# Performance work log

Measured on AMD Instinct MI355X. Metric: run time of the kernel, lower is better.

## Reference

```python
import jax, jax.numpy as jnp
import numpy as np

B, L_IN, T = 1024, 512, 96
IN_DIM, OUT_DIM = 1, 1
H_ENC, H_DEC = 128, 256  # decoder hidden = 2 * encoder hidden (bidir concat)


def _lstm_cell(x, h, c, Wih, Whh, b):
    # PyTorch gate order: i, f, g, o. b = b_ih + b_hh (equivalent to two biases).
    gates = x @ Wih.T + h @ Whh.T + b
    i, f, g, o = jnp.split(gates, 4, axis=-1)
    c = jax.nn.sigmoid(f) * c + jax.nn.sigmoid(i) * jnp.tanh(g)
    h = jax.nn.sigmoid(o) * jnp.tanh(c)
    return h, c


def _lstm_final(xs, Wih, Whh, b, hidden, reverse=False):
    # xs: [L, B, D]; returns final (h, c) only (encoder outputs are unused).
    h0 = jnp.zeros((xs.shape[1], hidden), xs.dtype)
    c0 = jnp.zeros((xs.shape[1], hidden), xs.dtype)

    def step(carry, x):
        h, c = _lstm_cell(x, carry[0], carry[1], Wih, Whh, b)
        return (h, c), None

    (h, c), _ = jax.lax.scan(step, (h0, c0), xs, reverse=reverse)
    return h, c


def setup_inputs() -> dict:
    key = jax.random.key(0)
    ks = jax.random.split(key, 13)
    p = lambda k, s: (jax.random.normal(k, s, jnp.float32) * 0.05)
    return {
        "source": jax.random.normal(ks[0], (B, L_IN, IN_DIM), jnp.float32),
        "target_tensor": jnp.zeros((B, T, OUT_DIM), jnp.float32),
        "enc_Wih_f": p(ks[1], (4 * H_ENC, IN_DIM)),
        "enc_Whh_f": p(ks[2], (4 * H_ENC, H_ENC)),
        "enc_b_f": p(ks[3], (4 * H_ENC,)),
        "enc_Wih_b": p(ks[4], (4 * H_ENC, IN_DIM)),
        "enc_Whh_b": p(ks[5], (4 * H_ENC, H_ENC)),
        "enc_b_b": p(ks[6], (4 * H_ENC,)),
        "dec_Wih": p(ks[7], (4 * H_DEC, OUT_DIM)),
        "dec_Whh": p(ks[8], (4 * H_DEC, H_DEC)),
        "dec_b": p(ks[9], (4 * H_DEC,)),
        "out_W": p(ks[10], (OUT_DIM, H_DEC)),
        "out_b": p(ks[11], (OUT_DIM,)),
    }


def reference(source, target_tensor, enc_Wih_f, enc_Whh_f, enc_b_f,
              enc_Wih_b, enc_Whh_b, enc_b_b,
              dec_Wih, dec_Whh, dec_b, out_W, out_b):
    batch = source.shape[0]
    t_len = target_tensor.shape[1]
    out_dim = target_tensor.shape[-1]

    xs = jnp.swapaxes(source, 0, 1)  # [L, B, IN]
    h_f, c_f = _lstm_final(xs, enc_Wih_f, enc_Whh_f, enc_b_f, H_ENC, reverse=False)
    h_b, c_b = _lstm_final(xs, enc_Wih_b, enc_Whh_b, enc_b_b, H_ENC, reverse=True)
    h0 = jnp.concatenate([h_f, h_b], axis=-1)  # [B, 2*H_ENC]
    c0 = jnp.concatenate([c_f, c_b], axis=-1)

    y0 = jnp.zeros((batch, out_dim), source.dtype)

    def dec_step(carry, _):
        h, c, y = carry
        h, c = _lstm_cell(y, h, c, dec_Wih, dec_Whh, dec_b)
        y = h @ out_W.T + out_b
        return (h, c, y), y

    _, ys = jax.lax.scan(dec_step, (h0, c0, y0), None, length=t_len)
    return jnp.swapaxes(ys, 0, 1)  # [B, T, OUT]
```

## Files before the change

### kernel.cpp

```cpp
#include <hip/hip_runtime.h>
#include <math.h>

#define H_ENC 128
#define H_DEC 256
#define L_SRC 512
#define T_DEC 96
#define B_TOT 1024

typedef _Float16 half8 __attribute__((ext_vector_type(8)));
typedef float f32x4 __attribute__((ext_vector_type(4)));

#define MFMA16(A, B, C) __builtin_amdgcn_mfma_f32_16x16x32_f16((A), (B), (C), 0, 0, 0)

__device__ __forceinline__ unsigned packu(float a, float b) {
    union { _Float16 h[2]; unsigned u; } x; x.h[0] = (_Float16)a; x.h[1] = (_Float16)b; return x.u;
}

__device__ __forceinline__ float sigmoidf_(float x) {
    return __builtin_amdgcn_rcpf(1.f + __expf(-x));
}
__device__ __forceinline__ float tanhf_(float x) {
    return 1.f - 2.f * __builtin_amdgcn_rcpf(__expf(2.f * x) + 1.f);
}

#define CNT_STRIDE 104
__global__ void zero_cnt(int* cnt) {
    int i = blockIdx.x * blockDim.x + threadIdx.x;
    if (i < 64 * CNT_STRIDE) cnt[i] = 0;
}

#define EB 4
#define HPAD 136
__global__ __launch_bounds__(512, 4)
void encoder_eb4r(
    const float* __restrict__ source,
    const float* __restrict__ Wih_f, const float* __restrict__ Whh_f, const float* __restrict__ b_f,
    const float* __restrict__ Wih_b, const float* __restrict__ Whh_b, const float* __restrict__ b_b,
    float* __restrict__ h0, float* __restrict__ c0)
{
    const int dir = blockIdx.x & 1;
    const int bg  = blockIdx.x >> 1;
    const int t   = threadIdx.x;
    const int w   = t >> 6;
    const int l   = t & 63;
    const int col = l & 15;
    const int grp = l >> 4;

    const float* Wih = dir ? Wih_b : Wih_f;
    const float* Whh = dir ? Whh_b : Whh_f;
    const float* bb  = dir ? b_b   : b_f;

    __shared__ float    xsT[L_SRC][EB];
    __shared__ _Float16 hbuf[2][EB][HPAD];
    __shared__ float    gbuf[4][EB][H_ENC];

    {
        const float* srcb = source + (size_t)bg * EB * L_SRC;
        for (int i = t; i < EB * L_SRC; i += 512) {
            int b = i >> 9, st = i & 511;
            xsT[st][b] = srcb[i];
        }
        for (int i = t; i < 2 * EB * HPAD; i += 512)
            ((_Float16*)hbuf)[i] = (_Float16)0.f;
    }

    half8 wf[4][4];
    #pragma unroll
    for (int tau = 0; tau < 4; ++tau) {
        const int n = 4 * w + tau;
        const int grow = (n >> 3) * H_ENC + 16 * (n & 7) + col;
        const float* wr = Whh + (size_t)grow * H_ENC;
        #pragma unroll
        for (int kt = 0; kt < 4; ++kt) {
            const float* p = wr + 32 * kt + 8 * grp;
            float4 v0 = *reinterpret_cast<const float4*>(p);
            float4 v1 = *reinterpret_cast<const float4*>(p + 4);
            half8 h;
            h[0] = (_Float16)v0.x; h[1] = (_Float16)v0.y; h[2] = (_Float16)v0.z; h[3] = (_Float16)v0.w;
            h[4] = (_Float16)v1.x; h[5] = (_Float16)v1.y; h[6] = (_Float16)v1.z; h[7] = (_Float16)v1.w;
            wf[tau][kt] = h;
        }
    }

    const int ub = t >> 7;
    const int ue = t & 127;
    const float bI = bb[ue],           wI = Wih[ue];
    const float bF = bb[H_ENC + ue],   wF = Wih[H_ENC + ue];
    const float bG = bb[2*H_ENC + ue], wG = Wih[2*H_ENC + ue];
    const float bO = bb[3*H_ENC + ue], wO = Wih[3*H_ENC + ue];

    float c = 0.f, hlast = 0.f;
    __syncthreads();

    int cur = 0;
    for (int s = 0; s < L_SRC; ++s) {
        const int step = dir ? (L_SRC - 1 - s) : s;

        half8 a0 = {0,0,0,0,0,0,0,0}, a1 = a0, a2 = a0, a3 = a0;
        if (col < EB) {
            a0 = *reinterpret_cast<const half8*>(&hbuf[cur][col][ 0 + 8 * grp]);
            a1 = *reinterpret_cast<const half8*>(&hbuf[cur][col][32 + 8 * grp]);
            a2 = *reinterpret_cast<const half8*>(&hbuf[cur][col][64 + 8 * grp]);
            a3 = *reinterpret_cast<const half8*>(&hbuf[cur][col][96 + 8 * grp]);
        }

        f32x4 acc0 = {0.f, 0.f, 0.f, 0.f};
        f32x4 acc1 = {0.f, 0.f, 0.f, 0.f};
        f32x4 acc2 = {0.f, 0.f, 0.f, 0.f};
        f32x4 acc3 = {0.f, 0.f, 0.f, 0.f};
        acc0 = MFMA16(a0, wf[0][0], acc0); acc0 = MFMA16(a1, wf[0][1], acc0);
        acc0 = MFMA16(a2, wf[0][2], acc0); acc0 = MFMA16(a3, wf[0][3], acc0);
        acc1 = MFMA16(a0, wf[1][0], acc1); acc1 = MFMA16(a1, wf[1][1], acc1);
        acc1 = MFMA16(a2, wf[1][2], acc1); acc1 = MFMA16(a3, wf[1][3], acc1);
        acc2 = MFMA16(a0, wf[2][0], acc2); acc2 = MFMA16(a1, wf[2][1], acc2);
        acc2 = MFMA16(a2, wf[2][2], acc2); acc2 = MFMA16(a3, wf[2][3], acc2);
        acc3 = MFMA16(a0, wf[3][0], acc3); acc3 = MFMA16(a1, wf[3][1], acc3);
        acc3 = MFMA16(a2, wf[3][2], acc3); acc3 = MFMA16(a3, wf[3][3], acc3);

        if (grp == 0) {
            #pragma unroll
            for (int tau = 0; tau < 4; ++tau) {
                const int n = 4 * w + tau;
                const int G = n >> 3;
                const int e = 16 * (n & 7) + col;
                const f32x4 acc = (tau == 0) ? acc0 : (tau == 1) ? acc1 : (tau == 2) ? acc2 : acc3;
                #pragma unroll
                for (int r = 0; r < 4; ++r)
                    gbuf[G][r][e] = acc[r];
            }
        }
        __syncthreads();

        {
            float x = xsT[step][ub];
            float gi = sigmoidf_(gbuf[0][ub][ue] + bI + wI * x);
            float gf = sigmoidf_(gbuf[1][ub][ue] + bF + wF * x);
            float gg = tanhf_  (gbuf[2][ub][ue] + bG + wG * x);
            float go = sigmoidf_(gbuf[3][ub][ue] + bO + wO * x);
            c = gf * c + gi * gg;
            float h = go * tanhf_(c);
            hlast = h;
            hbuf[cur ^ 1][ub][ue] = (_Float16)h;
        }
        __syncthreads();
        cur ^= 1;
    }

    h0[(size_t)(bg * EB + ub) * (2 * H_ENC) + dir * H_ENC + ue] = hlast;
    c0[(size_t)(bg * EB + ub) * (2 * H_ENC) + dir * H_ENC + ue] = c;
}

#define DB 16
__global__ __launch_bounds__(512, 2)
void decoder_split(
    const float* __restrict__ Wih,
    const float* __restrict__ bb,
    const float* __restrict__ outW,
    const float* __restrict__ outb,
    const float* __restrict__ h0,
    const float* __restrict__ c0,
    const float* __restrict__ Whh,
    unsigned* __restrict__ hx,
    int* __restrict__ cnt,
    float* __restrict__ out)
{
    const int blk = blockIdx.x;
    const int bg  = blk & 63;
    const int q   = blk >> 6;
    const int t   = threadIdx.x;
    const int w   = t >> 6;
    const int l   = t & 63;
    const int col = l & 15;
    const int grp = l >> 4;
    const int u   = w >> 1;
    const int fo  = w & 1;

    __shared__ unsigned hlU[DB][132];
    __shared__ float    exch[4][2][DB][16];
    __shared__ unsigned hnewU[DB][32];
    __shared__ float    yl[DB];
    __shared__ float    owl[H_DEC];
    int* mycnt = cnt + bg * CNT_STRIDE;

    if (t < H_DEC) owl[t] = outW[t];

    const int j0 = 64 * q + 16 * u + col;
    const int rA = (fo ? 256 : 0) + j0;
    const int rB = (fo ? 768 : 512) + j0;

    half8 wfA[8], wfB[8];
    #pragma unroll
    for (int kt = 0; kt < 8; ++kt) {
        const float* pa = Whh + (size_t)rA * H_DEC + 32 * kt + 8 * grp;
        const float* pb = Whh + (size_t)rB * H_DEC + 32 * kt + 8 * grp;
        float4 a0 = *reinterpret_cast<const float4*>(pa);
        float4 a1 = *reinterpret_cast<const float4*>(pa + 4);
        float4 b0 = *reinterpret_cast<const float4*>(pb);
        float4 b1 = *reinterpret_cast<const float4*>(pb + 4);
        half8 ha, hb;
        ha[0]=(_Float16)a0.x; ha[1]=(_Float16)a0.y; ha[2]=(_Float16)a0.z; ha[3]=(_Float16)a0.w;
        ha[4]=(_Float16)a1.x; ha[5]=(_Float16)a1.y; ha[6]=(_Float16)a1.z; ha[7]=(_Float16)a1.w;
        hb[0]=(_Float16)b0.x; hb[1]=(_Float16)b0.y; hb[2]=(_Float16)b0.z; hb[3]=(_Float16)b0.w;
        hb[4]=(_Float16)b1.x; hb[5]=(_Float16)b1.y; hb[6]=(_Float16)b1.z; hb[7]=(_Float16)b1.w;
        wfA[kt] = ha; wfB[kt] = hb;
    }

    const float bI = bb[j0],       wI = Wih[j0];
    const float bF = bb[256 + j0], wF = Wih[256 + j0];
    const float bG = bb[512 + j0], wG = Wih[512 + j0];
    const float bO = bb[768 + j0], wO = Wih[768 + j0];
    const float ob = outb[0];

    float c[4];
    #pragma unroll
    for (int r = 0; r < 4; ++r)
        c[r] = c0[(size_t)(bg * DB + 4 * grp + r) * H_DEC + j0];

    {
        int batch = t >> 5, pair = t & 31;
        int e = 64 * q + 2 * pair;
        const float* hp = h0 + (size_t)(bg * DB + batch) * H_DEC + e;
        unsigned v = packu(hp[0], hp[1]);
        __hip_atomic_store(&hx[(size_t)(bg * DB + batch) * 128 + 32 * q + pair], v,
                           __ATOMIC_RELAXED, __HIP_MEMORY_SCOPE_AGENT);
    }
    __syncthreads();
    if (t == 0) {
        __hip_atomic_fetch_add(&mycnt[0], 1, __ATOMIC_RELAXED, __HIP_MEMORY_SCOPE_AGENT);
        while (__hip_atomic_load(&mycnt[0], __ATOMIC_RELAXED, __HIP_MEMORY_SCOPE_AGENT) < 4)
            __builtin_amdgcn_s_sleep(1);
    }
    __syncthreads();

    for (int s = 1; s <= T_DEC; ++s) {
        const int rb = (s - 1) & 1, wb = s & 1;
        #pragma unroll
        for (int i = 0; i < 4; ++i) {
            int j = t + 512 * i;
            int batch = j >> 7, within = j & 127;
            unsigned v = __hip_atomic_load(
                &hx[(size_t)rb * (B_TOT * 128) + (size_t)(bg * DB + batch) * 128 + within],
                __ATOMIC_RELAXED, __HIP_MEMORY_SCOPE_AGENT);
            hlU[batch][within] = v;
        }
        __syncthreads();

        {
            int batch = t >> 5, seg = t & 31;
            half8 hv = *reinterpret_cast<const half8*>(
                reinterpret_cast<const char*>(hlU) + batch * 528 + seg * 16);
            float sum = 0.f;
            #pragma unroll
            for (int j = 0; j < 8; ++j) sum += (float)hv[j] * owl[8 * seg + j];
            #pragma unroll
            for (int m = 1; m < 32; m <<= 1) sum += __shfl_xor(sum, m);
            if (seg == 0) {
                float yv = sum + ob;
                yl[batch] = (s == 1) ? 0.f : yv;
                if (q == 0 && s >= 2) out[(size_t)(bg * DB + batch) * T_DEC + (s - 2)] = yv;
            }
        }

        half8 a[8];
        #pragma unroll
        for (int kt = 0; kt < 8; ++kt)
            a[kt] = *reinterpret_cast<const half8*>(
                reinterpret_cast<const char*>(hlU) + col * 528 + (32 * kt + 8 * grp) * 2);

        f32x4 accA = {0.f, 0.f, 0.f, 0.f};
        f32x4 accB = {0.f, 0.f, 0.f, 0.f};
        #pragma unroll
        for (int kt = 0; kt < 8; ++kt) {
            accA = MFMA16(a[kt], wfA[kt], accA);
            accB = MFMA16(a[kt], wfB[kt], accB);
        }

        if (fo) {
            #pragma unroll
            for (int r = 0; r < 4; ++r) {
                exch[u][0][4 * grp + r][col] = accA[r] + bF;
                exch[u][1][4 * grp + r][col] = accB[r] + bO;
            }
        }
        __syncthreads();

        if (!fo) {
            #pragma unroll
            for (int r = 0; r < 4; ++r) {
                float yb = yl[4 * grp + r];
                float gi = sigmoidf_(accA[r] + bI + wI * yb);
                float gg = tanhf_  (accB[r] + bG + wG * yb);
                float gf = sigmoidf_(exch[u][0][4 * grp + r][col] + wF * yb);
                float go = sigmoidf_(exch[u][1][4 * grp + r][col] + wO * yb);
                c[r] = gf * c[r] + gi * gg;
                float h = go * tanhf_(c[r]);
                reinterpret_cast<_Float16*>(hnewU)[(4 * grp + r) * 64 + 16 * u + col] = (_Float16)h;
            }
        }
        __syncthreads();

        {
            int batch = t >> 5, pair = t & 31;
            __hip_atomic_store(
                &hx[(size_t)wb * (B_TOT * 128) + (size_t)(bg * DB + batch) * 128 + 32 * q + pair],
                hnewU[batch][pair], __ATOMIC_RELAXED, __HIP_MEMORY_SCOPE_AGENT);
        }
        __syncthreads();
        if (t == 0) {
            __hip_atomic_fetch_add(&mycnt[s], 1, __ATOMIC_RELAXED, __HIP_MEMORY_SCOPE_AGENT);
            while (__hip_atomic_load(&mycnt[s], __ATOMIC_RELAXED, __HIP_MEMORY_SCOPE_AGENT) < 4)
                __builtin_amdgcn_s_sleep(1);
        }
        __syncthreads();
    }

    {
        #pragma unroll
        for (int i = 0; i < 4; ++i) {
            int j = t + 512 * i;
            int batch = j >> 7, within = j & 127;
            unsigned v = __hip_atomic_load(
                &hx[(size_t)(bg * DB + batch) * 128 + within],
                __ATOMIC_RELAXED, __HIP_MEMORY_SCOPE_AGENT);
            hlU[batch][within] = v;
        }
        __syncthreads();
        int batch = t >> 5, seg = t & 31;
        half8 hv = *reinterpret_cast<const half8*>(
            reinterpret_cast<const char*>(hlU) + batch * 528 + seg * 16);
        float sum = 0.f;
        #pragma unroll
        for (int j = 0; j < 8; ++j) sum += (float)hv[j] * owl[8 * seg + j];
        #pragma unroll
        for (int m = 1; m < 32; m <<= 1) sum += __shfl_xor(sum, m);
        if (q == 0 && seg == 0)
            out[(size_t)(bg * DB + batch) * T_DEC + (T_DEC - 1)] = sum + ob;
    }
}

extern "C" void kernel_launch(void* const* d_in, const int* in_sizes, int n_in,
                              void* d_out, int out_size, void* d_ws, size_t ws_size,
                              hipStream_t stream) {
    const float* source = (const float*)d_in[0];
    const float* eWih_f = (const float*)d_in[2];
    const float* eWhh_f = (const float*)d_in[3];
    const float* eb_f   = (const float*)d_in[4];
    const float* eWih_b = (const float*)d_in[5];
    const float* eWhh_b = (const float*)d_in[6];
    const float* eb_b   = (const float*)d_in[7];
    const float* dWih   = (const float*)d_in[8];
    const float* dWhh   = (const float*)d_in[9];
    const float* db     = (const float*)d_in[10];
    const float* oW     = (const float*)d_in[11];
    const float* obp    = (const float*)d_in[12];
    float* out = (float*)d_out;

    float*    h0  = (float*)d_ws;
    float*    c0  = h0 + (size_t)B_TOT * H_DEC;
    unsigned* hx  = (unsigned*)(c0 + (size_t)B_TOT * H_DEC);
    int*      cnt = (int*)(hx + (size_t)2 * B_TOT * 128);

    zero_cnt<<<(64 * CNT_STRIDE + 255) / 256, 256, 0, stream>>>(cnt);
    encoder_eb4r<<<256 * 2, 512, 0, stream>>>(
        source, eWih_f, eWhh_f, eb_f, eWih_b, eWhh_b, eb_b, h0, c0);
    decoder_split<<<256, 512, 0, stream>>>(
        dWih, db, oW, obp, h0, c0, dWhh, hx, cnt, out);
}
```

Measured before the change: 822.6 us.

## Process four batch chunks per decoder block and fold encoder bias into MFMA

The decoder now launches 64 blocks instead of 256, and each block loops over four 16-batch chunks that share the register-resident weight fragments. The cross-block counter barrier moves to the start of each step, so a block only waits before it reads hidden state. In the encoder, the bias is used as the initial MFMA accumulator instead of being added in the gate math. Both kernels raise wave priority around the MFMA chains. Fewer blocks lowers barrier and launch overhead but serialises four chunks per block, which may lengthen each step.

```diff
diff --git a/kernel.cpp b/kernel.cpp
--- a/kernel.cpp
+++ b/kernel.cpp
@@ -65,10 +65,12 @@
     }
 
     half8 wf[4][4];
+    float bias4[4];
     #pragma unroll
     for (int tau = 0; tau < 4; ++tau) {
         const int n = 4 * w + tau;
         const int grow = (n >> 3) * H_ENC + 16 * (n & 7) + col;
+        bias4[tau] = bb[grow];
         const float* wr = Whh + (size_t)grow * H_ENC;
         #pragma unroll
         for (int kt = 0; kt < 4; ++kt) {
@@ -84,10 +86,10 @@
 
     const int ub = t >> 7;
     const int ue = t & 127;
-    const float bI = bb[ue],           wI = Wih[ue];
-    const float bF = bb[H_ENC + ue],   wF = Wih[H_ENC + ue];
-    const float bG = bb[2*H_ENC + ue], wG = Wih[2*H_ENC + ue];
-    const float bO = bb[3*H_ENC + ue], wO = Wih[3*H_ENC + ue];
+    const float wI = Wih[ue];
+    const float wF = Wih[H_ENC + ue];
+    const float wG = Wih[2*H_ENC + ue];
+    const float wO = Wih[3*H_ENC + ue];
 
     float c = 0.f, hlast = 0.f;
     __syncthreads();
@@ -104,10 +106,11 @@
             a3 = *reinterpret_cast<const half8*>(&hbuf[cur][col][96 + 8 * grp]);
         }
 
-        f32x4 acc0 = {0.f, 0.f, 0.f, 0.f};
-        f32x4 acc1 = {0.f, 0.f, 0.f, 0.f};
-        f32x4 acc2 = {0.f, 0.f, 0.f, 0.f};
-        f32x4 acc3 = {0.f, 0.f, 0.f, 0.f};
+        f32x4 acc0 = {bias4[0], bias4[0], bias4[0], bias4[0]};
+        f32x4 acc1 = {bias4[1], bias4[1], bias4[1], bias4[1]};
+        f32x4 acc2 = {bias4[2], bias4[2], bias4[2], bias4[2]};
+        f32x4 acc3 = {bias4[3], bias4[3], bias4[3], bias4[3]};
+        __builtin_amdgcn_s_setprio(1);
         acc0 = MFMA16(a0, wf[0][0], acc0); acc0 = MFMA16(a1, wf[0][1], acc0);
         acc0 = MFMA16(a2, wf[0][2], acc0); acc0 = MFMA16(a3, wf[0][3], acc0);
         acc1 = MFMA16(a0, wf[1][0], acc1); acc1 = MFMA16(a1, wf[1][1], acc1);
@@ -116,6 +119,7 @@
         acc2 = MFMA16(a2, wf[2][2], acc2); acc2 = MFMA16(a3, wf[2][3], acc2);
         acc3 = MFMA16(a0, wf[3][0], acc3); acc3 = MFMA16(a1, wf[3][1], acc3);
         acc3 = MFMA16(a2, wf[3][2], acc3); acc3 = MFMA16(a3, wf[3][3], acc3);
+        __builtin_amdgcn_s_setprio(0);
 
         if (grp == 0) {
             #pragma unroll
@@ -133,10 +137,10 @@
 
         {
             float x = xsT[step][ub];
-            float gi = sigmoidf_(gbuf[0][ub][ue] + bI + wI * x);
-            float gf = sigmoidf_(gbuf[1][ub][ue] + bF + wF * x);
-            float gg = tanhf_  (gbuf[2][ub][ue] + bG + wG * x);
-            float go = sigmoidf_(gbuf[3][ub][ue] + bO + wO * x);
+            float gi = sigmoidf_(gbuf[0][ub][ue] + wI * x);
+            float gf = sigmoidf_(gbuf[1][ub][ue] + wF * x);
+            float gg = tanhf_  (gbuf[2][ub][ue] + wG * x);
+            float go = sigmoidf_(gbuf[3][ub][ue] + wO * x);
             c = gf * c + gi * gg;
             float h = go * tanhf_(c);
             hlast = h;
@@ -151,8 +155,9 @@
 }
 
 #define DB 16
+#define NCH 4
 __global__ __launch_bounds__(512, 2)
-void decoder_split(
+void decoder_mc(
     const float* __restrict__ Wih,
     const float* __restrict__ bb,
     const float* __restrict__ outW,
@@ -165,8 +170,8 @@
     float* __restrict__ out)
 {
     const int blk = blockIdx.x;
-    const int bg  = blk & 63;
-    const int q   = blk >> 6;
+    const int G2  = blk & 15;
+    const int q   = blk >> 4;
     const int t   = threadIdx.x;
     const int w   = t >> 6;
     const int l   = t & 63;
@@ -175,12 +180,12 @@
     const int u   = w >> 1;
     const int fo  = w & 1;
 
-    __shared__ unsigned hlU[DB][132];
+    __shared__ unsigned hlU[NCH][DB][132];
     __shared__ float    exch[4][2][DB][16];
     __shared__ unsigned hnewU[DB][32];
-    __shared__ float    yl[DB];
+    __shared__ float    yl[NCH][DB];
     __shared__ float    owl[H_DEC];
-    int* mycnt = cnt + bg * CNT_STRIDE;
+    int* mycnt = cnt + (size_t)(G2 * NCH) * CNT_STRIDE;
 
     if (t < H_DEC) owl[t] = outW[t];
 
@@ -211,12 +216,18 @@
     const float bO = bb[768 + j0], wO = Wih[768 + j0];
     const float ob = outb[0];
 
-    float c[4];
-    #pragma unroll
-    for (int r = 0; r < 4; ++r)
-        c[r] = c0[(size_t)(bg * DB + 4 * grp + r) * H_DEC + j0];
-
-    {
+    float c[NCH][4];
+    #pragma unroll
+    for (int ch = 0; ch < NCH; ++ch) {
+        const int bg = G2 * NCH + ch;
+        #pragma unroll
+        for (int r = 0; r < 4; ++r)
+            c[ch][r] = c0[(size_t)(bg * DB + 4 * grp + r) * H_DEC + j0];
+    }
+
+    #pragma unroll
+    for (int ch = 0; ch < NCH; ++ch) {
+        const int bg = G2 * NCH + ch;
         int batch = t >> 5, pair = t & 31;
         int e = 64 * q + 2 * pair;
         const float* hp = h0 + (size_t)(bg * DB + batch) * H_DEC + e;
@@ -225,116 +236,131 @@
                            __ATOMIC_RELAXED, __HIP_MEMORY_SCOPE_AGENT);
     }
     __syncthreads();
-    if (t == 0) {
-        __hip_atomic_fetch_add(&mycnt[0], 1, __ATOMIC_RELAXED, __HIP_MEMORY_SCOPE_AGENT);
-        while (__hip_atomic_load(&mycnt[0], __ATOMIC_RELAXED, __HIP_MEMORY_SCOPE_AGENT) < 4)
-            __builtin_amdgcn_s_sleep(1);
-    }
-    __syncthreads();
+    if (t < NCH)
+        __hip_atomic_fetch_add(&mycnt[(size_t)t * CNT_STRIDE + 0], 1,
+                               __ATOMIC_RELAXED, __HIP_MEMORY_SCOPE_AGENT);
 
     for (int s = 1; s <= T_DEC; ++s) {
         const int rb = (s - 1) & 1, wb = s & 1;
-        #pragma unroll
-        for (int i = 0; i < 4; ++i) {
-            int j = t + 512 * i;
-            int batch = j >> 7, within = j & 127;
-            unsigned v = __hip_atomic_load(
-                &hx[(size_t)rb * (B_TOT * 128) + (size_t)(bg * DB + batch) * 128 + within],
-                __ATOMIC_RELAXED, __HIP_MEMORY_SCOPE_AGENT);
-            hlU[batch][within] = v;
-        }
-        __syncthreads();
-
-        {
+
+        if (t < NCH) {
+            while (__hip_atomic_load(&mycnt[(size_t)t * CNT_STRIDE + (s - 1)],
+                                     __ATOMIC_RELAXED, __HIP_MEMORY_SCOPE_AGENT) < 4)
+                __builtin_amdgcn_s_sleep(1);
+        }
+        __syncthreads();
+
+        #pragma unroll
+        for (int i = 0; i < 16; ++i) {
+            int idx = t + 512 * i;
+            ((unsigned*)hlU)[(idx >> 7) * 132 + (idx & 127)] =
+                __hip_atomic_load(&hx[(size_t)rb * (B_TOT * 128) + (size_t)G2 * 8192 + idx],
+                                  __ATOMIC_RELAXED, __HIP_MEMORY_SCOPE_AGENT);
+        }
+        __syncthreads();
+
+        #pragma unroll
+        for (int ch = 0; ch < NCH; ++ch) {
+            const int bg = G2 * NCH + ch;
+            const char* hbase = reinterpret_cast<const char*>(hlU[ch]);
+
+            {
+                int batch = t >> 5, seg = t & 31;
+                half8 hv = *reinterpret_cast<const half8*>(hbase + batch * 528 + seg * 16);
+                float sum = 0.f;
+                #pragma unroll
+                for (int j = 0; j < 8; ++j) sum += (float)hv[j] * owl[8 * seg + j];
+                #pragma unroll
+                for (int m = 1; m < 32; m <<= 1) sum += __shfl_xor(sum, m);
+                if (seg == 0) {
+                    float yv = sum + ob;
+                    yl[ch][batch] = (s == 1) ? 0.f : yv;
+                    if (q == 0 && s >= 2) out[(size_t)(bg * DB + batch) * T_DEC + (s - 2)] = yv;
+                }
+            }
+
+            half8 a[8];
+            #pragma unroll
+            for (int kt = 0; kt < 8; ++kt)
+                a[kt] = *reinterpret_cast<const half8*>(hbase + col * 528 + (32 * kt + 8 * grp) * 2);
+
+            f32x4 accA = {0.f, 0.f, 0.f, 0.f};
+            f32x4 accB = {0.f, 0.f, 0.f, 0.f};
+            __builtin_amdgcn_s_setprio(1);
+            #pragma unroll
+            for (int kt = 0; kt < 8; ++kt) {
+                accA = MFMA16(a[kt], wfA[kt], accA);
+                accB = MFMA16(a[kt], wfB[kt], accB);
+            }
+            __builtin_amdgcn_s_setprio(0);
+
+            if (fo) {
+                #pragma unroll
+                for (int r = 0; r < 4; ++r) {
+                    exch[u][0][4 * grp + r][col] = accA[r] + bF;
+                    exch[u][1][4 * grp + r][col] = accB[r] + bO;
+                }
+            }
+            __syncthreads();
+
+            if (!fo) {
+                #pragma unroll
+                for (int r = 0; r < 4; ++r) {
+                    float yb = yl[ch][4 * grp + r];
+                    float gi = sigmoidf_(accA[r] + bI + wI * yb);
+                    float gg = tanhf_  (accB[r] + bG + wG * yb);
+                    float gf = sigmoidf_(exch[u][0][4 * grp + r][col] + wF * yb);
+                    float go = sigmoidf_(exch[u][1][4 * grp + r][col] + wO * yb);
+                    c[ch][r] = gf * c[ch][r] + gi * gg;
+                    float h = go * tanhf_(c[ch][r]);
+                    reinterpret_cast<_Float16*>(hnewU)[(4 * grp + r) * 64 + 16 * u + col] = (_Float16)h;
+                }
+            }
+            __syncthreads();
+
+            {
+                int batch = t >> 5, pair = t & 31;
+                __hip_atomic_store(
+                    &hx[(size_t)wb * (B_TOT * 128) + (size_t)(bg * DB + batch) * 128 + 32 * q + pair],
+                    hnewU[batch][pair], __ATOMIC_RELAXED, __HIP_MEMORY_SCOPE_AGENT);
+            }
+        }
+
+        __syncthreads();
+        if (t < NCH)
+            __hip_atomic_fetch_add(&mycnt[(size_t)t * CNT_STRIDE + s], 1,
+                                   __ATOMIC_RELAXED, __HIP_MEMORY_SCOPE_AGENT);
+    }
+
+    if (t < NCH) {
+        while (__hip_atomic_load(&mycnt[(size_t)t * CNT_STRIDE + T_DEC],
+                                 __ATOMIC_RELAXED, __HIP_MEMORY_SCOPE_AGENT) < 4)
+            __builtin_amdgcn_s_sleep(1);
+    }
+    __syncthreads();
+    #pragma unroll
+    for (int i = 0; i < 16; ++i) {
+        int idx = t + 512 * i;
+        ((unsigned*)hlU)[(idx >> 7) * 132 + (idx & 127)] =
+            __hip_atomic_load(&hx[(size_t)G2 * 8192 + idx],
+                              __ATOMIC_RELAXED, __HIP_MEMORY_SCOPE_AGENT);
+    }
+    __syncthreads();
+    if (q == 0) {
+        #pragma unroll
+        for (int ch = 0; ch < NCH; ++ch) {
+            const int bg = G2 * NCH + ch;
             int batch = t >> 5, seg = t & 31;
             half8 hv = *reinterpret_cast<const half8*>(
-                reinterpret_cast<const char*>(hlU) + batch * 528 + seg * 16);
+                reinterpret_cast<const char*>(hlU[ch]) + batch * 528 + seg * 16);
             float sum = 0.f;
             #pragma unroll
             for (int j = 0; j < 8; ++j) sum += (float)hv[j] * owl[8 * seg + j];
             #pragma unroll
             for (int m = 1; m < 32; m <<= 1) sum += __shfl_xor(sum, m);
-            if (seg == 0) {
-                float yv = sum + ob;
-                yl[batch] = (s == 1) ? 0.f : yv;
-                if (q == 0 && s >= 2) out[(size_t)(bg * DB + batch) * T_DEC + (s - 2)] = yv;
-            }
-        }
-
-        half8 a[8];
-        #pragma unroll
-        for (int kt = 0; kt < 8; ++kt)
-            a[kt] = *reinterpret_cast<const half8*>(
-                reinterpret_cast<const char*>(hlU) + col * 528 + (32 * kt + 8 * grp) * 2);
-
-        f32x4 accA = {0.f, 0.f, 0.f, 0.f};
-        f32x4 accB = {0.f, 0.f, 0.f, 0.f};
-        #pragma unroll
-        for (int kt = 0; kt < 8; ++kt) {
-            accA = MFMA16(a[kt], wfA[kt], accA);
-            accB = MFMA16(a[kt], wfB[kt], accB);
-        }
-
-        if (fo) {
-            #pragma unroll
-            for (int r = 0; r < 4; ++r) {
-                exch[u][0][4 * grp + r][col] = accA[r] + bF;
-                exch[u][1][4 * grp + r][col] = accB[r] + bO;
-            }
-        }
-        __syncthreads();
-
-        if (!fo) {
-            #pragma unroll
-            for (int r = 0; r < 4; ++r) {
-                float yb = yl[4 * grp + r];
-                float gi = sigmoidf_(accA[r] + bI + wI * yb);
-                float gg = tanhf_  (accB[r] + bG + wG * yb);
-                float gf = sigmoidf_(exch[u][0][4 * grp + r][col] + wF * yb);
-                float go = sigmoidf_(exch[u][1][4 * grp + r][col] + wO * yb);
-                c[r] = gf * c[r] + gi * gg;
-                float h = go * tanhf_(c[r]);
-                reinterpret_cast<_Float16*>(hnewU)[(4 * grp + r) * 64 + 16 * u + col] = (_Float16)h;
-            }
-        }
-        __syncthreads();
-
-        {
-            int batch = t >> 5, pair = t & 31;
-            __hip_atomic_store(
-                &hx[(size_t)wb * (B_TOT * 128) + (size_t)(bg * DB + batch) * 128 + 32 * q + pair],
-                hnewU[batch][pair], __ATOMIC_RELAXED, __HIP_MEMORY_SCOPE_AGENT);
-        }
-        __syncthreads();
-        if (t == 0) {
-            __hip_atomic_fetch_add(&mycnt[s], 1, __ATOMIC_RELAXED, __HIP_MEMORY_SCOPE_AGENT);
-            while (__hip_atomic_load(&mycnt[s], __ATOMIC_RELAXED, __HIP_MEMORY_SCOPE_AGENT) < 4)
-                __builtin_amdgcn_s_sleep(1);
-        }
-        __syncthreads();
-    }
-
-    {
-        #pragma unroll
-        for (int i = 0; i < 4; ++i) {
-            int j = t + 512 * i;
-            int batch = j >> 7, within = j & 127;
-            unsigned v = __hip_atomic_load(
-                &hx[(size_t)(bg * DB + batch) * 128 + within],
-                __ATOMIC_RELAXED, __HIP_MEMORY_SCOPE_AGENT);
-            hlU[batch][within] = v;
-        }
-        __syncthreads();
-        int batch = t >> 5, seg = t & 31;
-        half8 hv = *reinterpret_cast<const half8*>(
-            reinterpret_cast<const char*>(hlU) + batch * 528 + seg * 16);
-        float sum = 0.f;
-        #pragma unroll
-        for (int j = 0; j < 8; ++j) sum += (float)hv[j] * owl[8 * seg + j];
-        #pragma unroll
-        for (int m = 1; m < 32; m <<= 1) sum += __shfl_xor(sum, m);
-        if (q == 0 && seg == 0)
-            out[(size_t)(bg * DB + batch) * T_DEC + (T_DEC - 1)] = sum + ob;
+            if (seg == 0)
+                out[(size_t)(bg * DB + batch) * T_DEC + (T_DEC - 1)] = sum + ob;
+        }
     }
 }
 
@@ -363,6 +389,6 @@
     zero_cnt<<<(64 * CNT_STRIDE + 255) / 256, 256, 0, stream>>>(cnt);
     encoder_eb4r<<<256 * 2, 512, 0, stream>>>(
         source, eWih_f, eWhh_f, eb_f, eWih_b, eWhh_b, eb_b, h0, c0);
-    decoder_split<<<256, 512, 0, stream>>>(
+    decoder_mc<<<64, 512, 0, stream>>>(
         dWih, db, oW, obp, h0, c0, dWhh, hx, cnt, out);
 }
```

New measurement: 1.441 ms. +75.2%, slower.

## Remap encoder gates per wave so cell update uses shuffles instead of LDS

Applied to the files above, without the earlier changes.

Reorganizes the encoder so each wave computes all four gates (i,f,g,o) for the same 16 hidden units, then redistributes the MFMA accumulators with lane shuffles. This removes the gbuf shared-memory round trip and one __syncthreads per timestep. The bias is folded into the accumulator init, and each block now handles 8 batch rows instead of 4, halving the grid to 256 blocks. Fewer blocks may leave CUs underused, and the occupancy hint was dropped.

```diff
diff --git a/kernel.cpp b/kernel.cpp
--- a/kernel.cpp
+++ b/kernel.cpp
@@ -29,10 +29,10 @@
     if (i < 64 * CNT_STRIDE) cnt[i] = 0;
 }
 
-#define EB 4
+#define EB 8
 #define HPAD 136
-__global__ __launch_bounds__(512, 4)
-void encoder_eb4r(
+__global__ __launch_bounds__(512)
+void encoder_swz(
     const float* __restrict__ source,
     const float* __restrict__ Wih_f, const float* __restrict__ Whh_f, const float* __restrict__ b_f,
     const float* __restrict__ Wih_b, const float* __restrict__ Whh_b, const float* __restrict__ b_b,
@@ -52,7 +52,6 @@
 
     __shared__ float    xsT[L_SRC][EB];
     __shared__ _Float16 hbuf[2][EB][HPAD];
-    __shared__ float    gbuf[4][EB][H_ENC];
 
     {
         const float* srcb = source + (size_t)bg * EB * L_SRC;
@@ -64,11 +63,14 @@
             ((_Float16*)hbuf)[i] = (_Float16)0.f;
     }
 
+    const int e = 16 * w + col;
+
     half8 wf[4][4];
+    float bias4[4];
     #pragma unroll
-    for (int tau = 0; tau < 4; ++tau) {
-        const int n = 4 * w + tau;
-        const int grow = (n >> 3) * H_ENC + 16 * (n & 7) + col;
+    for (int tt = 0; tt < 4; ++tt) {
+        const int grow = tt * H_ENC + e;
+        bias4[tt] = bb[grow];
         const float* wr = Whh + (size_t)grow * H_ENC;
         #pragma unroll
         for (int kt = 0; kt < 4; ++kt) {
@@ -78,18 +80,22 @@
             half8 h;
             h[0] = (_Float16)v0.x; h[1] = (_Float16)v0.y; h[2] = (_Float16)v0.z; h[3] = (_Float16)v0.w;
             h[4] = (_Float16)v1.x; h[5] = (_Float16)v1.y; h[6] = (_Float16)v1.z; h[7] = (_Float16)v1.w;
-            wf[tau][kt] = h;
-        }
-    }
-
-    const int ub = t >> 7;
-    const int ue = t & 127;
-    const float bI = bb[ue],           wI = Wih[ue];
-    const float bF = bb[H_ENC + ue],   wF = Wih[H_ENC + ue];
-    const float bG = bb[2*H_ENC + ue], wG = Wih[2*H_ENC + ue];
-    const float bO = bb[3*H_ENC + ue], wO = Wih[3*H_ENC + ue];
-
-    float c = 0.f, hlast = 0.f;
+            wf[tt][kt] = h;
+        }
+    }
+
+    const int par  = grp & 1;
+    const int half = l >> 5;
+    const int bA   = 4 * half + 2 * par;
+    const int bB   = bA + 1;
+    const int src  = col + (half << 4);
+
+    const float wI = Wih[e];
+    const float wF = Wih[H_ENC + e];
+    const float wG = Wih[2 * H_ENC + e];
+    const float wO = Wih[3 * H_ENC + e];
+
+    float cA = 0.f, cB = 0.f, hAl = 0.f, hBl = 0.f;
     __syncthreads();
 
     int cur = 0;
@@ -104,10 +110,10 @@
             a3 = *reinterpret_cast<const half8*>(&hbuf[cur][col][96 + 8 * grp]);
         }
 
-        f32x4 acc0 = {0.f, 0.f, 0.f, 0.f};
-        f32x4 acc1 = {0.f, 0.f, 0.f, 0.f};
-        f32x4 acc2 = {0.f, 0.f, 0.f, 0.f};
-        f32x4 acc3 = {0.f, 0.f, 0.f, 0.f};
+        f32x4 acc0 = {bias4[0], bias4[0], bias4[0], bias4[0]};
+        f32x4 acc1 = {bias4[1], bias4[1], bias4[1], bias4[1]};
+        f32x4 acc2 = {bias4[2], bias4[2], bias4[2], bias4[2]};
+        f32x4 acc3 = {bias4[3], bias4[3], bias4[3], bias4[3]};
         acc0 = MFMA16(a0, wf[0][0], acc0); acc0 = MFMA16(a1, wf[0][1], acc0);
         acc0 = MFMA16(a2, wf[0][2], acc0); acc0 = MFMA16(a3, wf[0][3], acc0);
         acc1 = MFMA16(a0, wf[1][0], acc1); acc1 = MFMA16(a1, wf[1][1], acc1);
@@ -117,37 +123,42 @@
         acc3 = MFMA16(a0, wf[3][0], acc3); acc3 = MFMA16(a1, wf[3][1], acc3);
         acc3 = MFMA16(a2, wf[3][2], acc3); acc3 = MFMA16(a3, wf[3][3], acc3);
 
-        if (grp == 0) {
-            #pragma unroll
-            for (int tau = 0; tau < 4; ++tau) {
-                const int n = 4 * w + tau;
-                const int G = n >> 3;
-                const int e = 16 * (n & 7) + col;
-                const f32x4 acc = (tau == 0) ? acc0 : (tau == 1) ? acc1 : (tau == 2) ? acc2 : acc3;
-                #pragma unroll
-                for (int r = 0; r < 4; ++r)
-                    gbuf[G][r][e] = acc[r];
-            }
-        }
-        __syncthreads();
+        float i0 = __shfl(acc0[0], src), i1 = __shfl(acc0[1], src),
+              i2 = __shfl(acc0[2], src), i3 = __shfl(acc0[3], src);
+        float f0 = __shfl(acc1[0], src), f1 = __shfl(acc1[1], src),
+              f2 = __shfl(acc1[2], src), f3 = __shfl(acc1[3], src);
+        float g0 = __shfl(acc2[0], src), g1 = __shfl(acc2[1], src),
+              g2 = __shfl(acc2[2], src), g3 = __shfl(acc2[3], src);
+        float o0 = __shfl(acc3[0], src), o1 = __shfl(acc3[1], src),
+              o2 = __shfl(acc3[2], src), o3 = __shfl(acc3[3], src);
+        float iA = par ? i2 : i0, iB = par ? i3 : i1;
+        float fA = par ? f2 : f0, fB = par ? f3 : f1;
+        float gA = par ? g2 : g0, gB = par ? g3 : g1;
+        float oA = par ? o2 : o0, oB = par ? o3 : o1;
 
         {
-            float x = xsT[step][ub];
-            float gi = sigmoidf_(gbuf[0][ub][ue] + bI + wI * x);
-            float gf = sigmoidf_(gbuf[1][ub][ue] + bF + wF * x);
-            float gg = tanhf_  (gbuf[2][ub][ue] + bG + wG * x);
-            float go = sigmoidf_(gbuf[3][ub][ue] + bO + wO * x);
-            c = gf * c + gi * gg;
-            float h = go * tanhf_(c);
-            hlast = h;
-            hbuf[cur ^ 1][ub][ue] = (_Float16)h;
+            float xA = xsT[step][bA];
+            float xB = xsT[step][bB];
+            float giA = sigmoidf_(iA + wI * xA), giB = sigmoidf_(iB + wI * xB);
+            float gfA = sigmoidf_(fA + wF * xA), gfB = sigmoidf_(fB + wF * xB);
+            float ggA = tanhf_  (gA + wG * xA), ggB = tanhf_  (gB + wG * xB);
+            float goA = sigmoidf_(oA + wO * xA), goB = sigmoidf_(oB + wO * xB);
+            cA = gfA * cA + giA * ggA;
+            cB = gfB * cB + giB * ggB;
+            float hA = goA * tanhf_(cA);
+            float hB = goB * tanhf_(cB);
+            hAl = hA; hBl = hB;
+            hbuf[cur ^ 1][bA][e] = (_Float16)hA;
+            hbuf[cur ^ 1][bB][e] = (_Float16)hB;
         }
         __syncthreads();
         cur ^= 1;
     }
 
-    h0[(size_t)(bg * EB + ub) * (2 * H_ENC) + dir * H_ENC + ue] = hlast;
-    c0[(size_t)(bg * EB + ub) * (2 * H_ENC) + dir * H_ENC + ue] = c;
+    h0[(size_t)(bg * EB + bA) * (2 * H_ENC) + dir * H_ENC + e] = hAl;
+    c0[(size_t)(bg * EB + bA) * (2 * H_ENC) + dir * H_ENC + e] = cA;
+    h0[(size_t)(bg * EB + bB) * (2 * H_ENC) + dir * H_ENC + e] = hBl;
+    c0[(size_t)(bg * EB + bB) * (2 * H_ENC) + dir * H_ENC + e] = cB;
 }
 
 #define DB 16
@@ -361,7 +372,7 @@
     int*      cnt = (int*)(hx + (size_t)2 * B_TOT * 128);
 
     zero_cnt<<<(64 * CNT_STRIDE + 255) / 256, 256, 0, stream>>>(cnt);
-    encoder_eb4r<<<256 * 2, 512, 0, stream>>>(
+    encoder_swz<<<128 * 2, 512, 0, stream>>>(
         source, eWih_f, eWhh_f, eb_f, eWih_b, eWhh_b, eb_b, h0, c0);
     decoder_split<<<256, 512, 0, stream>>>(
         dWih, db, oW, obp, h0, c0, dWhh, hx, cnt, out);
```

After: 745.0 us, median of 2. 1.1x faster.
